# Performance work log

Hardware: AMD Instinct MI355X
Metric: run time of the kernel (lower is better)

The kernel has to match this reference:

```python
import jax, jax.numpy as jnp
import numpy as np

NUM_EMBEDDING = 512
EMBEDDING_DIM = 64
COMMITMENT_COST = 0.25


def setup_inputs() -> dict:
    key = jax.random.key(0)
    k1, k2 = jax.random.split(key)
    inputs = jax.random.normal(k1, (32, EMBEDDING_DIM, 64, 64), dtype=jnp.float32)
    # nn.Embedding weight init: uniform(-1/K, 1/K)
    weight = jax.random.uniform(
        k2, (NUM_EMBEDDING, EMBEDDING_DIM), dtype=jnp.float32,
        minval=-1.0 / NUM_EMBEDDING, maxval=1.0 / NUM_EMBEDDING)
    return {"inputs": inputs, "weight": weight}


def reference(inputs, weight):
    B, C, H, W = inputs.shape  # C == EMBEDDING_DIM
    K = weight.shape[0]
    sg = jax.lax.stop_gradient

    # NCHW -> NHWC -> [N, D]
    x = jnp.transpose(inputs, (0, 2, 3, 1)).reshape(-1, C)

    distances = (jnp.sum(x * x, axis=1, keepdims=True)
                 + jnp.sum(weight * weight, axis=1)
                 - 2.0 * jnp.matmul(x, weight.T))
    encoding_indices = jnp.argmin(distances, axis=1)  # [N]

    # one-hot scatter, as in the original
    encodings = jax.nn.one_hot(encoding_indices, K, dtype=x.dtype)  # [N, K]
    # quantized = encodings @ E  (== gather E[idx])
    quantized = jnp.matmul(encodings, weight)  # [N, D]

    q_latent_loss = jnp.mean((sg(quantized) - x) ** 2)
    e_latent_loss = jnp.mean((quantized - sg(x)) ** 2)
    loss = q_latent_loss + COMMITMENT_COST * e_latent_loss

    # straight-through estimator
    quantized_st = x + sg(quantized - x)

    avg_probs = jnp.mean(encodings, axis=0)  # [K]
    perplexity = jnp.exp(-jnp.sum(avg_probs * jnp.log(avg_probs + 1e-10)))

    # [N, D] -> [B, H, W, D] -> [B, D, H, W]
    quantized_out = jnp.transpose(quantized_st.reshape(B, H, W, C), (0, 3, 1, 2))
    return loss, quantized_out, perplexity, encodings
```

## Files before the change

kernel.cpp:

```cpp
#include <hip/hip_runtime.h>

#define BHW 262144
#define OUT_Q_OFF 1
#define OUT_P_OFF 8388609
#define OUT_E_OFF 8388610


typedef __attribute__((ext_vector_type(8))) short short8;
typedef __attribute__((ext_vector_type(4))) float f32x4;

__device__ __forceinline__ unsigned short f2bf(float f) {
    union { float f; unsigned u; } c; c.f = f;
    unsigned r = (c.u + 0x7FFFu + ((c.u >> 16) & 1u)) >> 16;
    return (unsigned short)r;
}

__global__ __launch_bounds__(512) void vq_init(const float* __restrict__ W, float* __restrict__ ws) {
    const int tid = blockIdx.x * 512 + threadIdx.x;
    if (tid < 512) {
        const float4* W4 = (const float4*)W;
        float s = 0.f;
#pragma unroll
        for (int i = 0; i < 16; ++i) {
            float4 v = W4[tid * 16 + i];
            s = fmaf(v.x, v.x, s); s = fmaf(v.y, v.y, s);
            s = fmaf(v.z, v.z, s); s = fmaf(v.w, v.w, s);
        }
        ws[513 + tid] = s;
    } else {
        const int c  = tid - 512;
        const int l  = c & 63;
        const int j  = (c >> 6) & 1;
        const int tn = c >> 7;
        const int n  = tn * 16 + (l & 15);
        const int k0 = j * 32 + ((l >> 4) & 3) * 8;
        const float* src = W + n * 64 + k0;
        unsigned h0 = f2bf(src[0]) | ((unsigned)f2bf(src[1]) << 16);
        unsigned h1 = f2bf(src[2]) | ((unsigned)f2bf(src[3]) << 16);
        unsigned h2 = f2bf(src[4]) | ((unsigned)f2bf(src[5]) << 16);
        unsigned h3 = f2bf(src[6]) | ((unsigned)f2bf(src[7]) << 16);
        uint4* dst = (uint4*)(ws + 1032);
        dst[c] = make_uint4(h0, h1, h2, h3);
    }
}

__global__ __launch_bounds__(256) void vq_main(const float* __restrict__ X,
                                               const float* __restrict__ W,
                                               float* __restrict__ out,
                                               float* __restrict__ ws) {
    const int t    = threadIdx.x;
    const int l    = t & 63;
    const int wv   = t >> 6;
    const int nlow = l & 15;
    const int kg   = l >> 4;
    const int rowbase = blockIdx.x * 64;
    const int b = rowbase >> 12;
    const int h = (rowbase >> 6) & 63;

    __shared__ int   best_lds[64];
    __shared__ float qlds[64][65];
    __shared__ float red[4];

    const float* xrow = X + (size_t)b * BHW + (size_t)h * 64 + wv * 16 + nlow;
    short8 a0, a1;
    {
        float tmp[16];
#pragma unroll
        for (int e = 0; e < 8; ++e) tmp[e]     = xrow[(size_t)(kg * 8 + e) * 4096];
#pragma unroll
        for (int e = 0; e < 8; ++e) tmp[8 + e] = xrow[(size_t)(32 + kg * 8 + e) * 4096];
#pragma unroll
        for (int e = 0; e < 8; ++e) { a0[e] = (short)f2bf(tmp[e]); a1[e] = (short)f2bf(tmp[8 + e]); }
    }

    const short8* __restrict__ B8  = (const short8*)(ws + 1032);
    const float*  __restrict__ wsq = ws + 513;
    float bS0 = 3.4e38f, bS1 = 3.4e38f, bS2 = 3.4e38f, bS3 = 3.4e38f;
    int   bK0 = 0, bK1 = 0, bK2 = 0, bK3 = 0;
#pragma unroll 2
    for (int tn = 0; tn < 32; ++tn) {
        short8 f0 = B8[tn * 128 + l];
        short8 f1 = B8[tn * 128 + 64 + l];
        f32x4 acc = {0.f, 0.f, 0.f, 0.f};
        acc = __builtin_amdgcn_mfma_f32_16x16x32_bf16(a0, f0, acc, 0, 0, 0);
        acc = __builtin_amdgcn_mfma_f32_16x16x32_bf16(a1, f1, acc, 0, 0, 0);
        const int   n  = tn * 16 + nlow;
        const float wq = wsq[n];
        float s;
        s = fmaf(-2.f, acc[0], wq); if (s < bS0) { bS0 = s; bK0 = n; }
        s = fmaf(-2.f, acc[1], wq); if (s < bS1) { bS1 = s; bK1 = n; }
        s = fmaf(-2.f, acc[2], wq); if (s < bS2) { bS2 = s; bK2 = n; }
        s = fmaf(-2.f, acc[3], wq); if (s < bS3) { bS3 = s; bK3 = n; }
    }
#pragma unroll
    for (int mask = 1; mask <= 8; mask <<= 1) {
        float oS; int oK;
        oS = __shfl_xor(bS0, mask); oK = __shfl_xor(bK0, mask);
        if (oS < bS0 || (oS == bS0 && oK < bK0)) { bS0 = oS; bK0 = oK; }
        oS = __shfl_xor(bS1, mask); oK = __shfl_xor(bK1, mask);
        if (oS < bS1 || (oS == bS1 && oK < bK1)) { bS1 = oS; bK1 = oK; }
        oS = __shfl_xor(bS2, mask); oK = __shfl_xor(bK2, mask);
        if (oS < bS2 || (oS == bS2 && oK < bK2)) { bS2 = oS; bK2 = oK; }
        oS = __shfl_xor(bS3, mask); oK = __shfl_xor(bK3, mask);
        if (oS < bS3 || (oS == bS3 && oK < bK3)) { bS3 = oS; bK3 = oK; }
    }
    if (nlow == 0) {
        best_lds[wv * 16 + kg * 4 + 0] = bK0;
        best_lds[wv * 16 + kg * 4 + 1] = bK1;
        best_lds[wv * 16 + kg * 4 + 2] = bK2;
        best_lds[wv * 16 + kg * 4 + 3] = bK3;
    }
    __syncthreads();

#pragma unroll
    for (int i = 0; i < 16; ++i) {
        int e = i * 256 + t;
        int row = e >> 6, d = e & 63;
        qlds[row][d] = W[best_lds[row] * 64 + d];
    }
    if (t < 64) atomicAdd((unsigned*)ws + 1 + best_lds[t], 1u);
    __syncthreads();

    const int dg = t >> 6;
    const int wq_ = t & 63;
    float lsum = 0.f;
    {
        const size_t base = (size_t)b * BHW + (size_t)h * 64 + wq_;
        const float* xp = X + base;
        float* op = out + OUT_Q_OFF + base;
#pragma unroll
        for (int i = 0; i < 16; ++i) {
            int d = dg * 16 + i;
            float x = xp[(size_t)d * 4096];
            float q = qlds[wq_][d];
            float diff = q - x;
            lsum = fmaf(diff, diff, lsum);
            op[(size_t)d * 4096] = x + diff;
        }
    }

    float2* enc2 = (float2*)(out + OUT_E_OFF);
    const size_t ebase = ((size_t)rowbase) << 8;
#pragma unroll 1
    for (int i = 0; i < 64; ++i) {
        int bk = best_lds[i];
        float2 v;
        v.x = (bk == 2 * t)     ? 1.f : 0.f;
        v.y = (bk == 2 * t + 1) ? 1.f : 0.f;
        enc2[ebase + ((size_t)i << 8) + t] = v;
    }

#pragma unroll
    for (int off = 32; off >= 1; off >>= 1) lsum += __shfl_down(lsum, off);
    if (l == 0) red[wv] = lsum;
    __syncthreads();
    if (t == 0) atomicAdd(ws, red[0] + red[1] + red[2] + red[3]);
}

__global__ __launch_bounds__(512) void vq_fin(const float* __restrict__ ws, float* __restrict__ out) {
    __shared__ float red[8];
    const int t = threadIdx.x;
    const unsigned* counts = (const unsigned*)ws + 1;
    float p = (float)counts[t] * (1.0f / 131072.0f);
    float s = p * logf(p + 1e-10f);
#pragma unroll
    for (int off = 32; off >= 1; off >>= 1) s += __shfl_down(s, off);
    if ((t & 63) == 0) red[t >> 6] = s;
    __syncthreads();
    if (t == 0) {
        float tot = 0.f;
#pragma unroll
        for (int i = 0; i < 8; ++i) tot += red[i];
        out[OUT_P_OFF] = expf(-tot);
        out[0] = ws[0] * (1.25f / 8388608.0f);
    }
}

extern "C" void kernel_launch(void* const* d_in, const int* in_sizes, int n_in,
                              void* d_out, int out_size, void* d_ws, size_t ws_size,
                              hipStream_t stream) {
    const float* X = (const float*)d_in[0];
    const float* W = (const float*)d_in[1];
    float* out = (float*)d_out;
    float* ws  = (float*)d_ws;

    hipMemsetAsync(d_ws, 0, 513 * sizeof(float), stream);
    vq_init<<<9, 512, 0, stream>>>(W, ws);
    vq_main<<<2048, 256, 0, stream>>>(X, W, out, ws);
    vq_fin<<<1, 512, 0, stream>>>(ws, out);
}
```

Baseline: 112.7 us.

## Split codebook across waves, keep x in registers, nontemporal output stores

Each wave now loads all 64 rows of x as MFMA A operands and scans only a quarter of the codebook. Per-wave argmin partials are merged through LDS. The wave's own x values are kept in registers and reused for the straight-through output, so x is not read a second time from global memory. The qlds gather is replaced by direct float4 reads of the chosen codebook rows. Outputs and the one-hot encodings are written with nontemporal stores, and launch bounds request 4 blocks per CU. The cost is more registers (four sets of A fragments and a 4x4 running best per thread) and an extra LDS merge step.

```diff
diff --git a/kernel.cpp b/kernel.cpp
--- a/kernel.cpp
+++ b/kernel.cpp
@@ -8,6 +8,7 @@
 
 typedef __attribute__((ext_vector_type(8))) short short8;
 typedef __attribute__((ext_vector_type(4))) float f32x4;
+typedef __attribute__((ext_vector_type(2))) float f32x2;
 
 __device__ __forceinline__ unsigned short f2bf(float f) {
     union { float f; unsigned u; } c; c.f = f;
@@ -44,10 +45,10 @@
     }
 }
 
-__global__ __launch_bounds__(256) void vq_main(const float* __restrict__ X,
-                                               const float* __restrict__ W,
-                                               float* __restrict__ out,
-                                               float* __restrict__ ws) {
+__global__ __launch_bounds__(256, 4) void vq_main(const float* __restrict__ X,
+                                                  const float* __restrict__ W,
+                                                  float* __restrict__ out,
+                                                  float* __restrict__ ws) {
     const int t    = threadIdx.x;
     const int l    = t & 63;
     const int wv   = t >> 6;
@@ -57,97 +58,121 @@
     const int b = rowbase >> 12;
     const int h = (rowbase >> 6) & 63;
 
+    __shared__ float partS[4][64];
+    __shared__ int   partK[4][64];
     __shared__ int   best_lds[64];
-    __shared__ float qlds[64][65];
     __shared__ float red[4];
 
-    const float* xrow = X + (size_t)b * BHW + (size_t)h * 64 + wv * 16 + nlow;
-    short8 a0, a1;
-    {
+    short8 a[4][2];
+    float  xf[16];
+    const float* xbase = X + (size_t)b * BHW + (size_t)h * 64 + nlow;
+#pragma unroll
+    for (int g = 0; g < 4; ++g) {
         float tmp[16];
-#pragma unroll
-        for (int e = 0; e < 8; ++e) tmp[e]     = xrow[(size_t)(kg * 8 + e) * 4096];
-#pragma unroll
-        for (int e = 0; e < 8; ++e) tmp[8 + e] = xrow[(size_t)(32 + kg * 8 + e) * 4096];
-#pragma unroll
-        for (int e = 0; e < 8; ++e) { a0[e] = (short)f2bf(tmp[e]); a1[e] = (short)f2bf(tmp[8 + e]); }
+        const float* xr = xbase + g * 16;
+#pragma unroll
+        for (int e = 0; e < 8; ++e) tmp[e]     = xr[(size_t)(kg * 8 + e) * 4096];
+#pragma unroll
+        for (int e = 0; e < 8; ++e) tmp[8 + e] = xr[(size_t)(32 + kg * 8 + e) * 4096];
+        short8 c0, c1;
+#pragma unroll
+        for (int e = 0; e < 8; ++e) { c0[e] = (short)f2bf(tmp[e]); c1[e] = (short)f2bf(tmp[8 + e]); }
+        a[g][0] = c0; a[g][1] = c1;
+        if (g == wv) {
+#pragma unroll
+            for (int e = 0; e < 16; ++e) xf[e] = tmp[e];
+        }
     }
 
     const short8* __restrict__ B8  = (const short8*)(ws + 1032);
     const float*  __restrict__ wsq = ws + 513;
-    float bS0 = 3.4e38f, bS1 = 3.4e38f, bS2 = 3.4e38f, bS3 = 3.4e38f;
-    int   bK0 = 0, bK1 = 0, bK2 = 0, bK3 = 0;
+    float bS[4][4];
+    int   bK[4][4];
+#pragma unroll
+    for (int g = 0; g < 4; ++g)
+#pragma unroll
+        for (int r = 0; r < 4; ++r) { bS[g][r] = 3.4e38f; bK[g][r] = 0; }
+
 #pragma unroll 2
-    for (int tn = 0; tn < 32; ++tn) {
-        short8 f0 = B8[tn * 128 + l];
-        short8 f1 = B8[tn * 128 + 64 + l];
-        f32x4 acc = {0.f, 0.f, 0.f, 0.f};
-        acc = __builtin_amdgcn_mfma_f32_16x16x32_bf16(a0, f0, acc, 0, 0, 0);
-        acc = __builtin_amdgcn_mfma_f32_16x16x32_bf16(a1, f1, acc, 0, 0, 0);
-        const int   n  = tn * 16 + nlow;
+    for (int tn = 0; tn < 8; ++tn) {
+        const int tni = wv * 8 + tn;
+        short8 f0 = B8[tni * 128 + l];
+        short8 f1 = B8[tni * 128 + 64 + l];
+        const int   n  = tni * 16 + nlow;
         const float wq = wsq[n];
-        float s;
-        s = fmaf(-2.f, acc[0], wq); if (s < bS0) { bS0 = s; bK0 = n; }
-        s = fmaf(-2.f, acc[1], wq); if (s < bS1) { bS1 = s; bK1 = n; }
-        s = fmaf(-2.f, acc[2], wq); if (s < bS2) { bS2 = s; bK2 = n; }
-        s = fmaf(-2.f, acc[3], wq); if (s < bS3) { bS3 = s; bK3 = n; }
-    }
-#pragma unroll
-    for (int mask = 1; mask <= 8; mask <<= 1) {
-        float oS; int oK;
-        oS = __shfl_xor(bS0, mask); oK = __shfl_xor(bK0, mask);
-        if (oS < bS0 || (oS == bS0 && oK < bK0)) { bS0 = oS; bK0 = oK; }
-        oS = __shfl_xor(bS1, mask); oK = __shfl_xor(bK1, mask);
-        if (oS < bS1 || (oS == bS1 && oK < bK1)) { bS1 = oS; bK1 = oK; }
-        oS = __shfl_xor(bS2, mask); oK = __shfl_xor(bK2, mask);
-        if (oS < bS2 || (oS == bS2 && oK < bK2)) { bS2 = oS; bK2 = oK; }
-        oS = __shfl_xor(bS3, mask); oK = __shfl_xor(bK3, mask);
-        if (oS < bS3 || (oS == bS3 && oK < bK3)) { bS3 = oS; bK3 = oK; }
-    }
-    if (nlow == 0) {
-        best_lds[wv * 16 + kg * 4 + 0] = bK0;
-        best_lds[wv * 16 + kg * 4 + 1] = bK1;
-        best_lds[wv * 16 + kg * 4 + 2] = bK2;
-        best_lds[wv * 16 + kg * 4 + 3] = bK3;
-    }
-    __syncthreads();
-
-#pragma unroll
-    for (int i = 0; i < 16; ++i) {
-        int e = i * 256 + t;
-        int row = e >> 6, d = e & 63;
-        qlds[row][d] = W[best_lds[row] * 64 + d];
-    }
-    if (t < 64) atomicAdd((unsigned*)ws + 1 + best_lds[t], 1u);
-    __syncthreads();
-
-    const int dg = t >> 6;
-    const int wq_ = t & 63;
+#pragma unroll
+        for (int g = 0; g < 4; ++g) {
+            f32x4 acc = {0.f, 0.f, 0.f, 0.f};
+            acc = __builtin_amdgcn_mfma_f32_16x16x32_bf16(a[g][0], f0, acc, 0, 0, 0);
+            acc = __builtin_amdgcn_mfma_f32_16x16x32_bf16(a[g][1], f1, acc, 0, 0, 0);
+#pragma unroll
+            for (int r = 0; r < 4; ++r) {
+                float s = fmaf(-2.f, acc[r], wq);
+                if (s < bS[g][r]) { bS[g][r] = s; bK[g][r] = n; }
+            }
+        }
+    }
+
+#pragma unroll
+    for (int g = 0; g < 4; ++g)
+#pragma unroll
+        for (int r = 0; r < 4; ++r) {
+            float s = bS[g][r]; int k = bK[g][r];
+#pragma unroll
+            for (int mask = 1; mask <= 8; mask <<= 1) {
+                float os = __shfl_xor(s, mask);
+                int   ok = __shfl_xor(k, mask);
+                if (os < s || (os == s && ok < k)) { s = os; k = ok; }
+            }
+            if (nlow == 0) {
+                partS[wv][g * 16 + kg * 4 + r] = s;
+                partK[wv][g * 16 + kg * 4 + r] = k;
+            }
+        }
+    __syncthreads();
+
+    if (t < 64) {
+        float s = partS[0][t]; int k = partK[0][t];
+#pragma unroll
+        for (int v = 1; v < 4; ++v) {
+            float os = partS[v][t]; int ok = partK[v][t];
+            if (os < s || (os == s && ok < k)) { s = os; k = ok; }
+        }
+        best_lds[t] = k;
+        atomicAdd((unsigned*)ws + 1 + k, 1u);
+    }
+    __syncthreads();
+
+    const int w_  = wv * 16 + nlow;
+    const int bk  = best_lds[w_];
+    const float4* W4 = (const float4*)W;
+    float4 q0 = W4[bk * 16 + kg * 2];
+    float4 q1 = W4[bk * 16 + kg * 2 + 1];
+    float4 q2 = W4[bk * 16 + 8 + kg * 2];
+    float4 q3 = W4[bk * 16 + 8 + kg * 2 + 1];
+    float qv[16] = {q0.x, q0.y, q0.z, q0.w, q1.x, q1.y, q1.z, q1.w,
+                    q2.x, q2.y, q2.z, q2.w, q3.x, q3.y, q3.z, q3.w};
     float lsum = 0.f;
-    {
-        const size_t base = (size_t)b * BHW + (size_t)h * 64 + wq_;
-        const float* xp = X + base;
-        float* op = out + OUT_Q_OFF + base;
-#pragma unroll
-        for (int i = 0; i < 16; ++i) {
-            int d = dg * 16 + i;
-            float x = xp[(size_t)d * 4096];
-            float q = qlds[wq_][d];
-            float diff = q - x;
-            lsum = fmaf(diff, diff, lsum);
-            op[(size_t)d * 4096] = x + diff;
-        }
-    }
-
-    float2* enc2 = (float2*)(out + OUT_E_OFF);
+    float* op = out + OUT_Q_OFF + (size_t)b * BHW + (size_t)h * 64 + w_;
+#pragma unroll
+    for (int e = 0; e < 8; ++e) {
+        float d0 = qv[e] - xf[e];
+        lsum = fmaf(d0, d0, lsum);
+        __builtin_nontemporal_store(xf[e] + d0, op + (size_t)(kg * 8 + e) * 4096);
+        float d1 = qv[8 + e] - xf[8 + e];
+        lsum = fmaf(d1, d1, lsum);
+        __builtin_nontemporal_store(xf[8 + e] + d1, op + (size_t)(32 + kg * 8 + e) * 4096);
+    }
+
+    f32x2* enc2 = (f32x2*)(out + OUT_E_OFF);
     const size_t ebase = ((size_t)rowbase) << 8;
 #pragma unroll 1
     for (int i = 0; i < 64; ++i) {
-        int bk = best_lds[i];
-        float2 v;
-        v.x = (bk == 2 * t)     ? 1.f : 0.f;
-        v.y = (bk == 2 * t + 1) ? 1.f : 0.f;
-        enc2[ebase + ((size_t)i << 8) + t] = v;
+        int bki = best_lds[i];
+        f32x2 v;
+        v.x = (bki == 2 * t)     ? 1.f : 0.f;
+        v.y = (bki == 2 * t + 1) ? 1.f : 0.f;
+        __builtin_nontemporal_store(v, enc2 + ebase + ((size_t)i << 8) + t);
     }
 
 #pragma unroll
@@ -184,7 +209,7 @@
     float* out = (float*)d_out;
     float* ws  = (float*)d_ws;
 
-    hipMemsetAsync(d_ws, 0, 513 * sizeof(float), stream);
+    (void)hipMemsetAsync(d_ws, 0, 513 * sizeof(float), stream);
     vq_init<<<9, 512, 0, stream>>>(W, ws);
     vq_main<<<2048, 256, 0, stream>>>(X, W, out, ws);
     vq_fin<<<1, 512, 0, stream>>>(ws, out);
```

Result: slower. 152.1 us (+35.0%).

## Restructure VQ main kernel to one wave per 16 rows, keep X in registers

Applied to the files above, without the earlier changes.

Each block is now a single 64-lane wave that handles 16 rows. It keeps its loaded X values in registers and reuses them for the loss and the straight-through output, so X is no longer reloaded and the LDS staging and barriers are gone. The codebook norm is folded into the MFMA accumulator init, and the -2 scale is pre-applied to the bf16 codebook, which removes the per-element FMA from the argmin loop. The loss atomics are spread across 256 slots that the final kernel reduces, which cuts contention on a single address. In exchange there are four times as many blocks, each with a smaller one-hot encoding write per lane group, and applying the -2 before bf16 rounding may change rounding slightly.

```diff
diff --git a/kernel.cpp b/kernel.cpp
--- a/kernel.cpp
+++ b/kernel.cpp
@@ -8,6 +8,7 @@
 
 typedef __attribute__((ext_vector_type(8))) short short8;
 typedef __attribute__((ext_vector_type(4))) float f32x4;
+typedef __attribute__((ext_vector_type(2))) float f32x2;
 
 __device__ __forceinline__ unsigned short f2bf(float f) {
     union { float f; unsigned u; } c; c.f = f;
@@ -26,7 +27,7 @@
             s = fmaf(v.x, v.x, s); s = fmaf(v.y, v.y, s);
             s = fmaf(v.z, v.z, s); s = fmaf(v.w, v.w, s);
         }
-        ws[513 + tid] = s;
+        ws[768 + tid] = s;
     } else {
         const int c  = tid - 512;
         const int l  = c & 63;
@@ -35,144 +36,132 @@
         const int n  = tn * 16 + (l & 15);
         const int k0 = j * 32 + ((l >> 4) & 3) * 8;
         const float* src = W + n * 64 + k0;
-        unsigned h0 = f2bf(src[0]) | ((unsigned)f2bf(src[1]) << 16);
-        unsigned h1 = f2bf(src[2]) | ((unsigned)f2bf(src[3]) << 16);
-        unsigned h2 = f2bf(src[4]) | ((unsigned)f2bf(src[5]) << 16);
-        unsigned h3 = f2bf(src[6]) | ((unsigned)f2bf(src[7]) << 16);
-        uint4* dst = (uint4*)(ws + 1032);
+        unsigned h0 = f2bf(-2.f * src[0]) | ((unsigned)f2bf(-2.f * src[1]) << 16);
+        unsigned h1 = f2bf(-2.f * src[2]) | ((unsigned)f2bf(-2.f * src[3]) << 16);
+        unsigned h2 = f2bf(-2.f * src[4]) | ((unsigned)f2bf(-2.f * src[5]) << 16);
+        unsigned h3 = f2bf(-2.f * src[6]) | ((unsigned)f2bf(-2.f * src[7]) << 16);
+        uint4* dst = (uint4*)(ws + 1280);
         dst[c] = make_uint4(h0, h1, h2, h3);
     }
 }
 
-__global__ __launch_bounds__(256) void vq_main(const float* __restrict__ X,
-                                               const float* __restrict__ W,
-                                               float* __restrict__ out,
-                                               float* __restrict__ ws) {
-    const int t    = threadIdx.x;
-    const int l    = t & 63;
-    const int wv   = t >> 6;
+__global__ __launch_bounds__(64) void vq_main(const float* __restrict__ X,
+                                              const float* __restrict__ W,
+                                              float* __restrict__ out,
+                                              float* __restrict__ ws) {
+    const int l    = threadIdx.x;
     const int nlow = l & 15;
     const int kg   = l >> 4;
-    const int rowbase = blockIdx.x * 64;
-    const int b = rowbase >> 12;
-    const int h = (rowbase >> 6) & 63;
+    const int rowbase = blockIdx.x * 16;
+    const int b  = rowbase >> 12;
+    const int h  = (rowbase >> 6) & 63;
+    const int w0 = rowbase & 63;
 
-    __shared__ int   best_lds[64];
-    __shared__ float qlds[64][65];
-    __shared__ float red[4];
+    const float* xr = X + (size_t)b * BHW + (size_t)h * 64 + (w0 + nlow);
+    float xf[16];
+#pragma unroll
+    for (int e = 0; e < 8; ++e) xf[e]     = xr[(size_t)(kg * 8 + e) * 4096];
+#pragma unroll
+    for (int e = 0; e < 8; ++e) xf[8 + e] = xr[(size_t)(32 + kg * 8 + e) * 4096];
+    short8 a0, a1;
+#pragma unroll
+    for (int e = 0; e < 8; ++e) { a0[e] = (short)f2bf(xf[e]); a1[e] = (short)f2bf(xf[8 + e]); }
 
-    const float* xrow = X + (size_t)b * BHW + (size_t)h * 64 + wv * 16 + nlow;
-    short8 a0, a1;
-    {
-        float tmp[16];
+    const short8* __restrict__ B8  = (const short8*)(ws + 1280);
+    const float*  __restrict__ wsq = ws + 768;
+    float bS[4]; int bK[4];
 #pragma unroll
-        for (int e = 0; e < 8; ++e) tmp[e]     = xrow[(size_t)(kg * 8 + e) * 4096];
-#pragma unroll
-        for (int e = 0; e < 8; ++e) tmp[8 + e] = xrow[(size_t)(32 + kg * 8 + e) * 4096];
-#pragma unroll
-        for (int e = 0; e < 8; ++e) { a0[e] = (short)f2bf(tmp[e]); a1[e] = (short)f2bf(tmp[8 + e]); }
-    }
+    for (int r = 0; r < 4; ++r) { bS[r] = 3.4e38f; bK[r] = 0; }
 
-    const short8* __restrict__ B8  = (const short8*)(ws + 1032);
-    const float*  __restrict__ wsq = ws + 513;
-    float bS0 = 3.4e38f, bS1 = 3.4e38f, bS2 = 3.4e38f, bS3 = 3.4e38f;
-    int   bK0 = 0, bK1 = 0, bK2 = 0, bK3 = 0;
 #pragma unroll 2
     for (int tn = 0; tn < 32; ++tn) {
         short8 f0 = B8[tn * 128 + l];
         short8 f1 = B8[tn * 128 + 64 + l];
-        f32x4 acc = {0.f, 0.f, 0.f, 0.f};
+        const float wq = wsq[tn * 16 + nlow];
+        f32x4 acc = {wq, wq, wq, wq};
         acc = __builtin_amdgcn_mfma_f32_16x16x32_bf16(a0, f0, acc, 0, 0, 0);
         acc = __builtin_amdgcn_mfma_f32_16x16x32_bf16(a1, f1, acc, 0, 0, 0);
-        const int   n  = tn * 16 + nlow;
-        const float wq = wsq[n];
-        float s;
-        s = fmaf(-2.f, acc[0], wq); if (s < bS0) { bS0 = s; bK0 = n; }
-        s = fmaf(-2.f, acc[1], wq); if (s < bS1) { bS1 = s; bK1 = n; }
-        s = fmaf(-2.f, acc[2], wq); if (s < bS2) { bS2 = s; bK2 = n; }
-        s = fmaf(-2.f, acc[3], wq); if (s < bS3) { bS3 = s; bK3 = n; }
+        const int n = tn * 16 + nlow;
+#pragma unroll
+        for (int r = 0; r < 4; ++r) {
+            if (acc[r] < bS[r]) { bS[r] = acc[r]; bK[r] = n; }
+        }
     }
 #pragma unroll
-    for (int mask = 1; mask <= 8; mask <<= 1) {
-        float oS; int oK;
-        oS = __shfl_xor(bS0, mask); oK = __shfl_xor(bK0, mask);
-        if (oS < bS0 || (oS == bS0 && oK < bK0)) { bS0 = oS; bK0 = oK; }
-        oS = __shfl_xor(bS1, mask); oK = __shfl_xor(bK1, mask);
-        if (oS < bS1 || (oS == bS1 && oK < bK1)) { bS1 = oS; bK1 = oK; }
-        oS = __shfl_xor(bS2, mask); oK = __shfl_xor(bK2, mask);
-        if (oS < bS2 || (oS == bS2 && oK < bK2)) { bS2 = oS; bK2 = oK; }
-        oS = __shfl_xor(bS3, mask); oK = __shfl_xor(bK3, mask);
-        if (oS < bS3 || (oS == bS3 && oK < bK3)) { bS3 = oS; bK3 = oK; }
-    }
-    if (nlow == 0) {
-        best_lds[wv * 16 + kg * 4 + 0] = bK0;
-        best_lds[wv * 16 + kg * 4 + 1] = bK1;
-        best_lds[wv * 16 + kg * 4 + 2] = bK2;
-        best_lds[wv * 16 + kg * 4 + 3] = bK3;
-    }
-    __syncthreads();
-
+    for (int r = 0; r < 4; ++r) {
 #pragma unroll
-    for (int i = 0; i < 16; ++i) {
-        int e = i * 256 + t;
-        int row = e >> 6, d = e & 63;
-        qlds[row][d] = W[best_lds[row] * 64 + d];
-    }
-    if (t < 64) atomicAdd((unsigned*)ws + 1 + best_lds[t], 1u);
-    __syncthreads();
-
-    const int dg = t >> 6;
-    const int wq_ = t & 63;
-    float lsum = 0.f;
-    {
-        const size_t base = (size_t)b * BHW + (size_t)h * 64 + wq_;
-        const float* xp = X + base;
-        float* op = out + OUT_Q_OFF + base;
-#pragma unroll
-        for (int i = 0; i < 16; ++i) {
-            int d = dg * 16 + i;
-            float x = xp[(size_t)d * 4096];
-            float q = qlds[wq_][d];
-            float diff = q - x;
-            lsum = fmaf(diff, diff, lsum);
-            op[(size_t)d * 4096] = x + diff;
+        for (int mask = 1; mask <= 8; mask <<= 1) {
+            float os = __shfl_xor(bS[r], mask);
+            int   ok = __shfl_xor(bK[r], mask);
+            if (os < bS[r] || (os == bS[r] && ok < bK[r])) { bS[r] = os; bK[r] = ok; }
         }
     }
 
-    float2* enc2 = (float2*)(out + OUT_E_OFF);
-    const size_t ebase = ((size_t)rowbase) << 8;
-#pragma unroll 1
-    for (int i = 0; i < 64; ++i) {
-        int bk = best_lds[i];
-        float2 v;
-        v.x = (bk == 2 * t)     ? 1.f : 0.f;
-        v.y = (bk == 2 * t + 1) ? 1.f : 0.f;
-        enc2[ebase + ((size_t)i << 8) + t] = v;
+    int rowBk = 0;
+    int myBk  = 0;
+    f32x2* encB = (f32x2*)(out + OUT_E_OFF);
+    const size_t Rbase = (size_t)rowbase;
+#pragma unroll
+    for (int m = 0; m < 16; ++m) {
+        int bkm = __shfl(bK[m & 3], (m >> 2) * 16);
+        if (nlow == m) rowBk = bkm;
+        if (l == m)    myBk = bkm;
+        f32x2* erow = encB + (Rbase + m) * 256;
+#pragma unroll
+        for (int c = 0; c < 4; ++c) {
+            int p = c * 64 + l;
+            f32x2 v;
+            v.x = (bkm == 2 * p)     ? 1.f : 0.f;
+            v.y = (bkm == 2 * p + 1) ? 1.f : 0.f;
+            erow[p] = v;
+        }
+    }
+    if (l < 16) atomicAdd((unsigned*)ws + 256 + myBk, 1u);
+
+    const float4* W4 = (const float4*)W;
+    float4 q0 = W4[rowBk * 16 + kg * 2];
+    float4 q1 = W4[rowBk * 16 + kg * 2 + 1];
+    float4 q2 = W4[rowBk * 16 + 8 + kg * 2];
+    float4 q3 = W4[rowBk * 16 + 8 + kg * 2 + 1];
+    float qv[16] = {q0.x, q0.y, q0.z, q0.w, q1.x, q1.y, q1.z, q1.w,
+                    q2.x, q2.y, q2.z, q2.w, q3.x, q3.y, q3.z, q3.w};
+    float lsum = 0.f;
+    float* op = out + OUT_Q_OFF + (size_t)b * BHW + (size_t)h * 64 + (w0 + nlow);
+#pragma unroll
+    for (int e = 0; e < 8; ++e) {
+        float d0 = qv[e] - xf[e];
+        lsum = fmaf(d0, d0, lsum);
+        op[(size_t)(kg * 8 + e) * 4096] = xf[e] + d0;
+        float d1 = qv[8 + e] - xf[8 + e];
+        lsum = fmaf(d1, d1, lsum);
+        op[(size_t)(32 + kg * 8 + e) * 4096] = xf[8 + e] + d1;
     }
 
 #pragma unroll
     for (int off = 32; off >= 1; off >>= 1) lsum += __shfl_down(lsum, off);
-    if (l == 0) red[wv] = lsum;
-    __syncthreads();
-    if (t == 0) atomicAdd(ws, red[0] + red[1] + red[2] + red[3]);
+    if (l == 0) atomicAdd(ws + (blockIdx.x & 255), lsum);
 }
 
 __global__ __launch_bounds__(512) void vq_fin(const float* __restrict__ ws, float* __restrict__ out) {
-    __shared__ float red[8];
+    __shared__ float redP[8], redL[8];
     const int t = threadIdx.x;
-    const unsigned* counts = (const unsigned*)ws + 1;
+    const unsigned* counts = (const unsigned*)ws + 256;
     float p = (float)counts[t] * (1.0f / 131072.0f);
     float s = p * logf(p + 1e-10f);
+    float lp = (t < 256) ? ws[t] : 0.f;
 #pragma unroll
-    for (int off = 32; off >= 1; off >>= 1) s += __shfl_down(s, off);
-    if ((t & 63) == 0) red[t >> 6] = s;
+    for (int off = 32; off >= 1; off >>= 1) {
+        s  += __shfl_down(s, off);
+        lp += __shfl_down(lp, off);
+    }
+    if ((t & 63) == 0) { redP[t >> 6] = s; redL[t >> 6] = lp; }
     __syncthreads();
     if (t == 0) {
-        float tot = 0.f;
+        float tp = 0.f, tl = 0.f;
 #pragma unroll
-        for (int i = 0; i < 8; ++i) tot += red[i];
-        out[OUT_P_OFF] = expf(-tot);
-        out[0] = ws[0] * (1.25f / 8388608.0f);
+        for (int i = 0; i < 8; ++i) { tp += redP[i]; tl += redL[i]; }
+        out[OUT_P_OFF] = expf(-tp);
+        out[0] = tl * (1.25f / 8388608.0f);
     }
 }
 
@@ -184,8 +173,8 @@
     float* out = (float*)d_out;
     float* ws  = (float*)d_ws;
 
-    hipMemsetAsync(d_ws, 0, 513 * sizeof(float), stream);
+    (void)hipMemsetAsync(d_ws, 0, 768 * sizeof(float), stream);
     vq_init<<<9, 512, 0, stream>>>(W, ws);
-    vq_main<<<2048, 256, 0, stream>>>(X, W, out, ws);
+    vq_main<<<8192, 64, 0, stream>>>(X, W, out, ws);
     vq_fin<<<1, 512, 0, stream>>>(ws, out);
 }
```

New measurement: 116.5 us. 3.4% more time.
